# Optimization experiments

Measured on AMD Instinct MI355X. Metric: run time of the kernel, lower is better.

The kernel has to match this reference:

```python
import jax, jax.numpy as jnp
import numpy as np

LOWER_HALF_WEIGHT = 2.0
UPPER_HALF_WEIGHT = 1.0
N = 33554432  # B*N flat elements
H_VAL = 256


def setup_inputs() -> dict:
    key = jax.random.key(0)
    k1, k2 = jax.random.split(key)
    d_out = jax.random.normal(k1, (N,), dtype=jnp.float32)
    height_indices = jax.random.randint(k2, (N,), 0, H_VAL, dtype=jnp.int64 if jax.config.jax_enable_x64 else jnp.int32)
    return {"d_out": d_out, "target": 1, "height_indices": height_indices, "H": H_VAL}


def reference(d_out, target, height_indices, H):
    mid_point = H // 2
    # vectorized replacement of the per-element Python loop
    weights = jnp.where(height_indices >= mid_point,
                        jnp.float32(LOWER_HALF_WEIGHT),
                        jnp.float32(UPPER_HALF_WEIGHT))
    t = jnp.float32(target)
    # BCEWithLogits (stable): max(x,0) - x*t + log(1 + exp(-|x|))
    x = d_out
    bce = jnp.maximum(x, 0.0) - x * t + jnp.log1p(jnp.exp(-jnp.abs(x)))
    return (bce * weights).mean()
```

## Files before the change

kernel.cpp:

```cpp
#include <hip/hip_runtime.h>

typedef float  float4v __attribute__((ext_vector_type(4)));
typedef int    int4v   __attribute__((ext_vector_type(4)));

__device__ __forceinline__ float scalar_as_float(const void* p) {
    int iv = *(const int*)p;
    if (iv >= -1000000 && iv <= 1000000) return (float)iv;
    return *(const float*)p;
}
__device__ __forceinline__ int scalar_as_int(const void* p) {
    int iv = *(const int*)p;
    if (iv >= -1000000 && iv <= 1000000) return iv;
    return (int)(*(const float*)p);
}

__device__ __forceinline__ float bce4(float4v xv, int4v iv, int mid, float t) {
    float s = 0.0f;
    #pragma unroll
    for (int j = 0; j < 4; ++j) {
        float xx = xv[j];
        float w  = (iv[j] >= mid) ? 2.0f : 1.0f;
        float a  = fabsf(xx);
        float bce = fmaxf(xx, 0.0f) - xx * t + __logf(1.0f + __expf(-a));
        s += w * bce;
    }
    return s;
}

__global__ __launch_bounds__(256) void rwl_partial_kernel(
        const float* __restrict__ x,
        const int*   __restrict__ idx,
        const void*  __restrict__ target_p,
        const void*  __restrict__ H_p,
        float* __restrict__ partials,
        int n_vec, int n_total)
{
    const float t   = scalar_as_float(target_p);
    const int   mid = scalar_as_int(H_p) >> 1;

    const int tid    = blockIdx.x * blockDim.x + threadIdx.x;
    const int stride = gridDim.x * blockDim.x;

    const float4v* __restrict__ xv4 = (const float4v*)x;
    const int4v*   __restrict__ iv4 = (const int4v*)idx;

    float acc0 = 0.0f, acc1 = 0.0f, acc2 = 0.0f, acc3 = 0.0f;

    int i = tid;
    for (; i + 3 * stride < n_vec; i += 4 * stride) {
        float4v x0 = xv4[i];
        float4v x1 = xv4[i + stride];
        float4v x2 = xv4[i + 2 * stride];
        float4v x3 = xv4[i + 3 * stride];
        int4v   i0 = iv4[i];
        int4v   i1 = iv4[i + stride];
        int4v   i2 = iv4[i + 2 * stride];
        int4v   i3 = iv4[i + 3 * stride];
        acc0 += bce4(x0, i0, mid, t);
        acc1 += bce4(x1, i1, mid, t);
        acc2 += bce4(x2, i2, mid, t);
        acc3 += bce4(x3, i3, mid, t);
    }
    for (; i < n_vec; i += stride)
        acc0 += bce4(xv4[i], iv4[i], mid, t);

    float acc = (acc0 + acc1) + (acc2 + acc3);

    if (tid == 0) {
        for (int k = n_vec * 4; k < n_total; ++k) {
            float xx = x[k];
            float w  = (idx[k] >= mid) ? 2.0f : 1.0f;
            float a  = fabsf(xx);
            acc += w * (fmaxf(xx, 0.0f) - xx * t + __logf(1.0f + __expf(-a)));
        }
    }

    #pragma unroll
    for (int off = 32; off > 0; off >>= 1)
        acc += __shfl_down(acc, off, 64);

    __shared__ float smem[4];
    const int lane = threadIdx.x & 63;
    const int wid  = threadIdx.x >> 6;
    if (lane == 0) smem[wid] = acc;
    __syncthreads();
    if (threadIdx.x == 0)
        partials[blockIdx.x] = smem[0] + smem[1] + smem[2] + smem[3];
}

__global__ __launch_bounds__(256) void rwl_final_kernel(
        const float* __restrict__ partials, int n, float inv_total,
        float* __restrict__ out)
{
    float acc = 0.0f;
    for (int i = threadIdx.x; i < n; i += 256) acc += partials[i];
    #pragma unroll
    for (int off = 32; off > 0; off >>= 1)
        acc += __shfl_down(acc, off, 64);
    __shared__ float smem[4];
    const int lane = threadIdx.x & 63;
    const int wid  = threadIdx.x >> 6;
    if (lane == 0) smem[wid] = acc;
    __syncthreads();
    if (threadIdx.x == 0)
        out[0] = (smem[0] + smem[1] + smem[2] + smem[3]) * inv_total;
}

extern "C" void kernel_launch(void* const* d_in, const int* in_sizes, int n_in,
                              void* d_out, int out_size, void* d_ws, size_t ws_size,
                              hipStream_t stream) {
    const float* x      = (const float*)d_in[0];
    const void*  target = d_in[1];
    const int*   idx    = (const int*)d_in[2];
    const void*  Hp     = d_in[3];
    float* out          = (float*)d_out;
    float* partials     = (float*)d_ws;

    const int n_total = in_sizes[0];
    const int n_vec   = n_total >> 2;

    int blocks = (n_vec + 1023) / 1024;
    if (blocks > 8192) blocks = 8192;
    if (blocks < 1)    blocks = 1;

    rwl_partial_kernel<<<blocks, 256, 0, stream>>>(
        x, idx, target, Hp, partials, n_vec, n_total);

    const float inv_total = 1.0f / (float)n_total;
    rwl_final_kernel<<<1, 256, 0, stream>>>(partials, blocks, inv_total, out);
}
```

Before: 290.5 us.

## Restructure reduction into per-wave contiguous chunks with fewer blocks

Each wavefront now reads one contiguous 256-vector chunk per iteration, issuing all four loads before a scheduling barrier and then computing. The grid is capped at 2048 blocks with a launch-bounds occupancy hint, and the per-element sum is reordered into a tree. The intent is more memory-level parallelism and locality for a bandwidth-bound streaming reduction. The trade-off is fewer waves in flight to hide latency, plus a tail loop whose indexing must cover the leftover elements correctly.

```diff
diff --git a/kernel.cpp b/kernel.cpp
--- a/kernel.cpp
+++ b/kernel.cpp
@@ -15,53 +15,54 @@
 }
 
 __device__ __forceinline__ float bce4(float4v xv, int4v iv, int mid, float t) {
-    float s = 0.0f;
+    float e[4];
     #pragma unroll
     for (int j = 0; j < 4; ++j) {
         float xx = xv[j];
         float w  = (iv[j] >= mid) ? 2.0f : 1.0f;
         float a  = fabsf(xx);
         float bce = fmaxf(xx, 0.0f) - xx * t + __logf(1.0f + __expf(-a));
-        s += w * bce;
+        e[j] = w * bce;
     }
-    return s;
+    return (e[0] + e[1]) + (e[2] + e[3]);
 }
 
-__global__ __launch_bounds__(256) void rwl_partial_kernel(
+__global__ __launch_bounds__(256, 4) void rwl_partial_kernel(
         const float* __restrict__ x,
         const int*   __restrict__ idx,
         const void*  __restrict__ target_p,
         const void*  __restrict__ H_p,
         float* __restrict__ partials,
-        int n_vec, int n_total)
+        int n_vec, int n_total, int n_super)
 {
     const float t   = scalar_as_float(target_p);
     const int   mid = scalar_as_int(H_p) >> 1;
 
-    const int tid    = blockIdx.x * blockDim.x + threadIdx.x;
-    const int stride = gridDim.x * blockDim.x;
+    const int lane = threadIdx.x & 63;
+    const int wid  = threadIdx.x >> 6;
+    const int gw   = blockIdx.x * (blockDim.x >> 6) + wid;
+    const int GW   = gridDim.x * (blockDim.x >> 6);
 
     const float4v* __restrict__ xv4 = (const float4v*)x;
     const int4v*   __restrict__ iv4 = (const int4v*)idx;
 
     float acc0 = 0.0f, acc1 = 0.0f, acc2 = 0.0f, acc3 = 0.0f;
 
-    int i = tid;
-    for (; i + 3 * stride < n_vec; i += 4 * stride) {
-        float4v x0 = xv4[i];
-        float4v x1 = xv4[i + stride];
-        float4v x2 = xv4[i + 2 * stride];
-        float4v x3 = xv4[i + 3 * stride];
-        int4v   i0 = iv4[i];
-        int4v   i1 = iv4[i + stride];
-        int4v   i2 = iv4[i + 2 * stride];
-        int4v   i3 = iv4[i + 3 * stride];
+    for (int s = 0; s < n_super; ++s) {
+        const int base = (s * GW + gw) * 256 + lane;
+        float4v x0 = xv4[base];        int4v i0 = iv4[base];
+        float4v x1 = xv4[base +  64];  int4v i1 = iv4[base +  64];
+        float4v x2 = xv4[base + 128];  int4v i2 = iv4[base + 128];
+        float4v x3 = xv4[base + 192];  int4v i3 = iv4[base + 192];
+        __builtin_amdgcn_sched_barrier(0);
         acc0 += bce4(x0, i0, mid, t);
         acc1 += bce4(x1, i1, mid, t);
         acc2 += bce4(x2, i2, mid, t);
         acc3 += bce4(x3, i3, mid, t);
     }
-    for (; i < n_vec; i += stride)
+
+    const int tid = blockIdx.x * blockDim.x + threadIdx.x;
+    for (int i = n_super * GW * 256 + tid; i < n_vec; i += GW * 64)
         acc0 += bce4(xv4[i], iv4[i], mid, t);
 
     float acc = (acc0 + acc1) + (acc2 + acc3);
@@ -80,8 +81,6 @@
         acc += __shfl_down(acc, off, 64);
 
     __shared__ float smem[4];
-    const int lane = threadIdx.x & 63;
-    const int wid  = threadIdx.x >> 6;
     if (lane == 0) smem[wid] = acc;
     __syncthreads();
     if (threadIdx.x == 0)
@@ -120,11 +119,15 @@
     const int n_vec   = n_total >> 2;
 
     int blocks = (n_vec + 1023) / 1024;
-    if (blocks > 8192) blocks = 8192;
+    if (blocks > 2048) blocks = 2048;
     if (blocks < 1)    blocks = 1;
 
+    const int GW      = blocks * 4;
+    const int chunk   = GW * 256;
+    const int n_super = n_vec / chunk;
+
     rwl_partial_kernel<<<blocks, 256, 0, stream>>>(
-        x, idx, target, Hp, partials, n_vec, n_total);
+        x, idx, target, Hp, partials, n_vec, n_total, n_super);
 
     const float inv_total = 1.0f / (float)n_total;
     rwl_final_kernel<<<1, 256, 0, stream>>>(partials, blocks, inv_total, out);
```

New measurement: 280.6 us. 3.4% less time.
